# Kernel tuning notes

Hardware: AMD Instinct MI355X
Metric: run time of the kernel (lower is better)

Reference implementation:

```python
import jax, jax.numpy as jnp
import numpy as np

B, L, D_WORD, D_TIME, POS_DIM = 16, 200, 64, 56, 8
T_DIM = D_WORD + D_TIME + POS_DIM  # 128 = transformer_dim
N_HEADS, D_K, D_V = 2, 64, 64
USER_SIZE = 20000
POS_VOCAB = 1000
PAD = 0
NEG_BIG = float(-(2 ** 32) + 1)


def _layer_norm(x, g, b, eps=1e-5):
    mu = jnp.mean(x, axis=-1, keepdims=True)
    var = jnp.var(x, axis=-1, keepdims=True)
    return (x - mu) * jax.lax.rsqrt(var + eps) * g + b


def setup_inputs() -> dict:
    key = jax.random.key(0)
    ks = jax.random.split(key, 16)

    def xn(k, shape, fan):
        # xavier_normal-like scale
        std = (2.0 / (shape[0] + shape[1])) ** 0.5
        return jax.random.normal(k, shape, dtype=jnp.float32) * std

    return {
        "input_embeddings": jax.random.normal(ks[0], (B, L, D_WORD), dtype=jnp.float32),
        "time_embedding": jax.random.normal(ks[1], (B, L, D_TIME), dtype=jnp.float32),
        "inputs": jax.random.randint(ks[2], (B, L), 0, USER_SIZE, dtype=jnp.int32),
        "pos_table": jax.random.normal(ks[3], (POS_VOCAB, POS_DIM), dtype=jnp.float32) * 0.02,
        "W_q": xn(ks[4], (T_DIM, N_HEADS * D_K), 0),
        "W_k": xn(ks[5], (T_DIM, N_HEADS * D_K), 0),
        "W_v": xn(ks[6], (T_DIM, N_HEADS * D_V), 0),
        "W_o": xn(ks[7], (N_HEADS * D_V, T_DIM), 0),
        "lin1_w": xn(ks[8], (T_DIM, T_DIM), 0),
        "lin1_b": jnp.zeros((T_DIM,), dtype=jnp.float32),
        "lin2_w": xn(ks[9], (T_DIM, T_DIM), 0),
        "lin2_b": jnp.zeros((T_DIM,), dtype=jnp.float32),
        "ln_g": jnp.ones((T_DIM,), dtype=jnp.float32),
        "ln_b": jnp.zeros((T_DIM,), dtype=jnp.float32),
        "pred_w": xn(ks[10], (T_DIM, USER_SIZE), 0),
        "pred_b": jnp.zeros((USER_SIZE,), dtype=jnp.float32),
    }


def _forward(input_embeddings, time_embedding, inputs, pos_table,
             W_q, W_k, W_v, W_o, lin1_w, lin1_b, lin2_w, lin2_b,
             ln_g, ln_b, pred_w, pred_b):
    bsz, q_len, _ = input_embeddings.shape
    pad_mask = (inputs == PAD)  # (B, L) query-row padding mask

    # user_lt_attention + merger reduce to identity residual path here (eval, no extra params)
    user_embedding = input_embeddings
    order_embed = pos_table[jnp.arange(q_len)]  # (L, 8)
    order_embed = jnp.broadcast_to(order_embed[None], (bsz, q_len, POS_DIM))
    x = jnp.concatenate([user_embedding, time_embedding, order_embed], axis=-1)  # (B,L,T_DIM)

    # multi-head attention (hand-rolled, same math as TransformerBlock)
    Qh = (x @ W_q).reshape(bsz, q_len, N_HEADS, D_K).transpose(0, 2, 1, 3)  # bhqd
    Kh = (x @ W_k).reshape(bsz, q_len, N_HEADS, D_K).transpose(0, 2, 1, 3)
    Vh = (x @ W_v).reshape(bsz, q_len, N_HEADS, D_V).transpose(0, 2, 1, 3)

    temperature = D_K ** 0.5 + 1e-6
    scores = jnp.einsum('bhqd,bhkd->bhqk', Qh, Kh) / temperature
    causal = jnp.triu(jnp.ones((q_len, q_len), dtype=bool), k=1)  # (L,L)
    mask_ = causal[None, None, :, :] | pad_mask[:, None, :, None]  # causal OR query-pad rows
    scores = jnp.where(mask_, NEG_BIG, scores)
    attn = jax.nn.softmax(scores, axis=-1)
    V_att = jnp.einsum('bhqk,bhkd->bhqd', attn, Vh)
    V_att = V_att.transpose(0, 2, 1, 3).reshape(bsz, q_len, N_HEADS * D_V)
    V_att = V_att @ W_o  # (B,L,T_DIM)

    X = _layer_norm(x + V_att, ln_g, ln_b)
    ffn = jax.nn.relu(X @ lin1_w + lin1_b) @ lin2_w + lin2_b
    att_out = _layer_norm(ffn + X, ln_g, ln_b)

    pred = att_out @ pred_w + pred_b  # (B, L, USER_SIZE)

    # previous-user mask: -inf at every user id already seen at or before step i
    seqs = jnp.broadcast_to(inputs[:, None, :], (bsz, q_len, q_len))  # seqs[b,i,j]=inputs[b,j]
    tril = jnp.tril(jnp.ones((q_len, q_len), dtype=inputs.dtype))
    idx = seqs * tril  # future positions -> index 0 (matches torch tril*seqs)
    idx = jnp.concatenate([idx, jnp.zeros((bsz, q_len, 1), dtype=inputs.dtype)], axis=-1)
    bi = jnp.arange(bsz)[:, None, None]
    li = jnp.arange(q_len)[None, :, None]
    prev_mask = jnp.zeros((bsz, q_len, USER_SIZE), dtype=pred.dtype).at[bi, li, idx].set(-jnp.inf)

    return pred + prev_mask


def reference(input_embeddings, time_embedding, inputs, pos_table,
              W_q, W_k, W_v, W_o, lin1_w, lin1_b, lin2_w, lin2_b,
              ln_g, ln_b, pred_w, pred_b):
    return _forward(input_embeddings, time_embedding, inputs, pos_table,
                    W_q, W_k, W_v, W_o, lin1_w, lin1_b, lin2_w, lin2_b,
                    ln_g, ln_b, pred_w, pred_b)
```

## Files before the change

kernel.cpp:

```cpp
#include <hip/hip_runtime.h>
#include <math.h>
#include <float.h>

#define BB_ 16
#define LL_ 200
#define TD 128
#define DK 64
#define NH 2
#define USER 20000
#define ROWS (BB_ * LL_)
#define NEG_BIG (-4294967295.0f)
#define MASK_NEG (-1.0e30f)

typedef unsigned short u16;
typedef __attribute__((ext_vector_type(8))) short bf16x8;
typedef __attribute__((ext_vector_type(4))) float f32x4;

__device__ __forceinline__ u16 f2bf(float f) {
    unsigned int u = __float_as_uint(f);
    u = (u + 0x7FFFu + ((u >> 16) & 1u)) >> 16;
    return (u16)u;
}

__global__ void qkv_kernel(const float* __restrict__ emb,
                           const float* __restrict__ tim,
                           const float* __restrict__ pos,
                           const float* __restrict__ Wq,
                           const float* __restrict__ Wk,
                           const float* __restrict__ Wv,
                           float* __restrict__ x,
                           float* __restrict__ q,
                           float* __restrict__ k,
                           float* __restrict__ v) {
    int r = blockIdx.x;
    int c = threadIdx.x;
    int b = r / LL_, l = r % LL_;
    __shared__ float xr[TD];
    float xv;
    if (c < 64)        xv = emb[r * 64 + c];
    else if (c < 120)  xv = tim[r * 56 + (c - 64)];
    else               xv = pos[l * 8 + (c - 120)];
    xr[c] = xv;
    x[r * TD + c] = xv;
    __syncthreads();
    float aq = 0.f, ak = 0.f, av = 0.f;
#pragma unroll 8
    for (int kk = 0; kk < TD; ++kk) {
        float xx = xr[kk];
        aq += xx * Wq[kk * TD + c];
        ak += xx * Wk[kk * TD + c];
        av += xx * Wv[kk * TD + c];
    }
    int h = c >> 6, d = c & 63;
    int base = ((b * NH + h) * LL_ + l) * DK + d;
    q[base] = aq; k[base] = ak; v[base] = av;
}

__global__ __launch_bounds__(256) void attn_kernel(const float* __restrict__ q,
                                                   const float* __restrict__ k,
                                                   const float* __restrict__ v,
                                                   const int* __restrict__ inputs,
                                                   float* __restrict__ vatt) {
    int blk = blockIdx.x;
    int bh = blk / LL_, qi = blk % LL_;
    int b = bh >> 1, h = bh & 1;
    int t = threadIdx.x;
    int w = t >> 6;
    __shared__ float4 qrow4[DK / 4];
    __shared__ float p[256];
    __shared__ float wmax[4], wsum[4];
    __shared__ float pvred[4][DK];

    if (t < DK / 4) qrow4[t] = ((const float4*)(q + (size_t)(bh * LL_ + qi) * DK))[t];
    __syncthreads();

    bool padq = (inputs[b * LL_ + qi] == 0);
    float s = -INFINITY;
    if (t < LL_) {
        if (t > qi || padq) {
            s = NEG_BIG;
        } else {
            const float4* kr = (const float4*)(k + (size_t)(bh * LL_ + t) * DK);
            float acc = 0.f;
#pragma unroll
            for (int d4 = 0; d4 < DK / 4; ++d4) {
                float4 kv = kr[d4], qv = qrow4[d4];
                acc = fmaf(qv.x, kv.x, fmaf(qv.y, kv.y,
                      fmaf(qv.z, kv.z, fmaf(qv.w, kv.w, acc))));
            }
            s = acc / 8.000001f;
        }
    }
    float m = s;
#pragma unroll
    for (int off = 32; off >= 1; off >>= 1) m = fmaxf(m, __shfl_xor(m, off));
    if ((t & 63) == 0) wmax[w] = m;
    __syncthreads();
    float mx = fmaxf(fmaxf(wmax[0], wmax[1]), fmaxf(wmax[2], wmax[3]));

    float e = (t < LL_) ? expf(s - mx) : 0.f;
    p[t] = e;
    float ss = e;
#pragma unroll
    for (int off = 32; off >= 1; off >>= 1) ss += __shfl_xor(ss, off);
    if ((t & 63) == 0) wsum[w] = ss;
    __syncthreads();
    float inv = 1.0f / ((wsum[0] + wsum[1]) + (wsum[2] + wsum[3]));

    int d = t & 63;
    const float* vb = v + ((size_t)(bh * LL_ + w * 50)) * DK + d;
    float acc = 0.f;
#pragma unroll 10
    for (int i = 0; i < 50; ++i)
        acc = fmaf(p[w * 50 + i], vb[(size_t)i * DK], acc);
    pvred[w][d] = acc;
    __syncthreads();
    if (t < DK) {
        float r = (pvred[0][t] + pvred[1][t]) + (pvred[2][t] + pvred[3][t]);
        vatt[(size_t)(b * LL_ + qi) * TD + h * DK + t] = r * inv;
    }
}

__device__ __forceinline__ float block_ln_128(float y, float* red, int c,
                                              const float* g, const float* bb) {
    red[c] = y; __syncthreads();
    for (int st = 64; st > 0; st >>= 1) {
        if (c < st) red[c] += red[c + st];
        __syncthreads();
    }
    float mu = red[0] * (1.0f / 128.0f);
    __syncthreads();
    float d = y - mu;
    red[c] = d * d; __syncthreads();
    for (int st = 64; st > 0; st >>= 1) {
        if (c < st) red[c] += red[c + st];
        __syncthreads();
    }
    float var = red[0] * (1.0f / 128.0f);
    __syncthreads();
    return d * (1.0f / sqrtf(var + 1e-5f)) * g[c] + bb[c];
}

__global__ void mlp_kernel(const float* __restrict__ vatt,
                           const float* __restrict__ x,
                           const float* __restrict__ Wo,
                           const float* __restrict__ l1w,
                           const float* __restrict__ l1b,
                           const float* __restrict__ l2w,
                           const float* __restrict__ l2b,
                           const float* __restrict__ g,
                           const float* __restrict__ bb,
                           u16* __restrict__ att_b) {
    int r = blockIdx.x;
    int c = threadIdx.x;
    __shared__ float vr[TD], Xs[TD], h1[TD], red[TD];
    vr[c] = vatt[r * TD + c];
    __syncthreads();
    float acc = 0.f;
#pragma unroll 8
    for (int kk = 0; kk < TD; ++kk) acc += vr[kk] * Wo[kk * TD + c];
    float y = acc + x[r * TD + c];
    float Xc = block_ln_128(y, red, c, g, bb);
    Xs[c] = Xc;
    __syncthreads();
    float a1 = l1b[c];
#pragma unroll 8
    for (int kk = 0; kk < TD; ++kk) a1 += Xs[kk] * l1w[kk * TD + c];
    h1[c] = fmaxf(a1, 0.f);
    __syncthreads();
    float a2 = l2b[c];
#pragma unroll 8
    for (int kk = 0; kk < TD; ++kk) a2 += h1[kk] * l2w[kk * TD + c];
    float z = a2 + Xc;
    att_b[r * TD + c] = f2bf(block_ln_128(z, red, c, g, bb));
}

__global__ __launch_bounds__(256) void pack_w(const float* __restrict__ W,
                                              u16* __restrict__ Bp) {
    int idx = blockIdx.x * 256 + threadIdx.x;
    int kb = idx / USER;
    int n  = idx - kb * USER;
    const float* wp = W + (size_t)kb * 8 * USER + n;
    bf16x8 vv;
#pragma unroll
    for (int j = 0; j < 8; ++j) vv[j] = (short)f2bf(wp[(size_t)j * USER]);
    *(bf16x8*)(Bp + (size_t)idx * 8) = vv;
}

__global__ __launch_bounds__(256) void pred_mfma(const u16* __restrict__ Ab,
                                                 const u16* __restrict__ Bp,
                                                 const float* __restrict__ bias,
                                                 float* __restrict__ out) {
    int wave = threadIdx.x >> 6;
    int lane = threadIdx.x & 63;
    int l15 = lane & 15, l4 = lane >> 4;
    int m0 = blockIdx.y * 64;
    int n0 = blockIdx.x * 256 + wave * 64;

    f32x4 acc[4][4];
#pragma unroll
    for (int mf = 0; mf < 4; ++mf)
#pragma unroll
        for (int nf = 0; nf < 4; ++nf)
            acc[mf][nf] = (f32x4){0.f, 0.f, 0.f, 0.f};

    const u16* Aptr = Ab + (size_t)(m0 + l15) * TD + l4 * 8;

#pragma unroll
    for (int ks = 0; ks < 4; ++ks) {
        bf16x8 a[4], b[4];
#pragma unroll
        for (int mf = 0; mf < 4; ++mf)
            a[mf] = *(const bf16x8*)(Aptr + mf * 16 * TD + ks * 32);
#pragma unroll
        for (int nf = 0; nf < 4; ++nf) {
            int col = n0 + nf * 16 + l15;
            if (col >= USER) col = USER - 1;
            b[nf] = *(const bf16x8*)(Bp + ((size_t)(ks * 4 + l4) * USER + col) * 8);
        }
#pragma unroll
        for (int mf = 0; mf < 4; ++mf)
#pragma unroll
            for (int nf = 0; nf < 4; ++nf)
                acc[mf][nf] = __builtin_amdgcn_mfma_f32_16x16x32_bf16(
                    b[nf], a[mf], acc[mf][nf], 0, 0, 0);
    }

#pragma unroll
    for (int nf = 0; nf < 4; ++nf) {
        int n = n0 + nf * 16 + l4 * 4;
        if (n < USER) {
            f32x4 bw = *(const f32x4*)(bias + n);
#pragma unroll
            for (int mf = 0; mf < 4; ++mf) {
                f32x4 val = acc[mf][nf];
                val.x += bw.x; val.y += bw.y; val.z += bw.z; val.w += bw.w;
                __builtin_nontemporal_store(val,
                    (f32x4*)(out + (size_t)(m0 + mf * 16 + l15) * USER + n));
            }
        }
    }
}

__global__ void mask_kernel(const int* __restrict__ inputs, float* __restrict__ out) {
    int r = blockIdx.x;
    int b = r / LL_, i = r % LL_;
    int t = threadIdx.x;
    float* row = out + (size_t)r * USER;
    if (t == 0) row[0] = MASK_NEG;
    for (int j = t; j <= i; j += 128) {
        int u = inputs[b * LL_ + j];
        row[u] = MASK_NEG;
    }
}

extern "C" void kernel_launch(void* const* d_in, const int* in_sizes, int n_in,
                              void* d_out, int out_size, void* d_ws, size_t ws_size,
                              hipStream_t stream) {
    const float* emb   = (const float*)d_in[0];
    const float* tim   = (const float*)d_in[1];
    const int*   inp   = (const int*)  d_in[2];
    const float* pos   = (const float*)d_in[3];
    const float* Wq    = (const float*)d_in[4];
    const float* Wk    = (const float*)d_in[5];
    const float* Wv    = (const float*)d_in[6];
    const float* Wo    = (const float*)d_in[7];
    const float* l1w   = (const float*)d_in[8];
    const float* l1b   = (const float*)d_in[9];
    const float* l2w   = (const float*)d_in[10];
    const float* l2b   = (const float*)d_in[11];
    const float* g     = (const float*)d_in[12];
    const float* bbeta = (const float*)d_in[13];
    const float* predw = (const float*)d_in[14];
    const float* predb = (const float*)d_in[15];
    float* out = (float*)d_out;

    float* ws   = (float*)d_ws;
    float* x    = ws;
    float* q    = x    + ROWS * TD;
    float* k    = q    + ROWS * TD;
    float* v    = k    + ROWS * TD;
    float* vatt = v    + ROWS * TD;
    u16* att_b  = (u16*)(vatt + ROWS * TD);
    u16* Wb     = att_b + ROWS * TD;

    hipLaunchKernelGGL(qkv_kernel, dim3(ROWS), dim3(TD), 0, stream,
                       emb, tim, pos, Wq, Wk, Wv, x, q, k, v);
    hipLaunchKernelGGL(attn_kernel, dim3(BB_ * NH * LL_), dim3(256), 0, stream,
                       q, k, v, inp, vatt);
    hipLaunchKernelGGL(mlp_kernel, dim3(ROWS), dim3(TD), 0, stream,
                       vatt, x, Wo, l1w, l1b, l2w, l2b, g, bbeta, att_b);
    hipLaunchKernelGGL(pack_w, dim3(16 * USER / 256), dim3(256), 0, stream,
                       predw, Wb);
    hipLaunchKernelGGL(pred_mfma, dim3((USER + 255) / 256, ROWS / 64), dim3(256), 0, stream,
                       att_b, Wb, predb, out);
    hipLaunchKernelGGL(mask_kernel, dim3(ROWS), dim3(TD), 0, stream,
                       inp, out);
}
```

Measured before the change: 470.3 us.

## Batch QKV rows per block, store K transposed, swap pred grid order

The QKV projection now handles 8 rows per block, so each weight load is reused across 8 rows instead of 1. K is written in a transposed layout so that in the attention score loop neighbouring threads read contiguous addresses across key positions. The prediction GEMM grid is reordered so the row-tile index varies fastest, which changes which weight and activation tiles sit in cache together. The change costs more registers in the QKV kernel and gives it fewer blocks. It also assumes 8-row groups never cross a batch boundary, which holds because 200 is divisible by 8.

```diff
diff --git a/kernel.cpp b/kernel.cpp
--- a/kernel.cpp
+++ b/kernel.cpp
@@ -9,6 +9,7 @@
 #define NH 2
 #define USER 20000
 #define ROWS (BB_ * LL_)
+#define QROWS 8
 #define NEG_BIG (-4294967295.0f)
 #define MASK_NEG (-1.0e30f)
 
@@ -22,7 +23,7 @@
     return (u16)u;
 }
 
-__global__ void qkv_kernel(const float* __restrict__ emb,
+__global__ __launch_bounds__(128) void qkv_kernel(const float* __restrict__ emb,
                            const float* __restrict__ tim,
                            const float* __restrict__ pos,
                            const float* __restrict__ Wq,
@@ -30,34 +31,54 @@
                            const float* __restrict__ Wv,
                            float* __restrict__ x,
                            float* __restrict__ q,
-                           float* __restrict__ k,
+                           float* __restrict__ kT,
                            float* __restrict__ v) {
-    int r = blockIdx.x;
+    int r0 = blockIdx.x * QROWS;
     int c = threadIdx.x;
-    int b = r / LL_, l = r % LL_;
-    __shared__ float xr[TD];
-    float xv;
-    if (c < 64)        xv = emb[r * 64 + c];
-    else if (c < 120)  xv = tim[r * 56 + (c - 64)];
-    else               xv = pos[l * 8 + (c - 120)];
-    xr[c] = xv;
-    x[r * TD + c] = xv;
-    __syncthreads();
-    float aq = 0.f, ak = 0.f, av = 0.f;
+    __shared__ float xr[QROWS][TD];
+#pragma unroll
+    for (int i = 0; i < QROWS; ++i) {
+        int r = r0 + i;
+        int l = r % LL_;
+        float xv;
+        if (c < 64)        xv = emb[r * 64 + c];
+        else if (c < 120)  xv = tim[r * 56 + (c - 64)];
+        else               xv = pos[l * 8 + (c - 120)];
+        xr[i][c] = xv;
+        x[r * TD + c] = xv;
+    }
+    __syncthreads();
+    float aq[QROWS], ak[QROWS], av[QROWS];
+#pragma unroll
+    for (int i = 0; i < QROWS; ++i) { aq[i] = 0.f; ak[i] = 0.f; av[i] = 0.f; }
 #pragma unroll 8
     for (int kk = 0; kk < TD; ++kk) {
-        float xx = xr[kk];
-        aq += xx * Wq[kk * TD + c];
-        ak += xx * Wk[kk * TD + c];
-        av += xx * Wv[kk * TD + c];
+        float wq = Wq[kk * TD + c], wk = Wk[kk * TD + c], wv = Wv[kk * TD + c];
+#pragma unroll
+        for (int i = 0; i < QROWS; ++i) {
+            float xx = xr[i][kk];
+            aq[i] = fmaf(xx, wq, aq[i]);
+            ak[i] = fmaf(xx, wk, ak[i]);
+            av[i] = fmaf(xx, wv, av[i]);
+        }
     }
     int h = c >> 6, d = c & 63;
-    int base = ((b * NH + h) * LL_ + l) * DK + d;
-    q[base] = aq; k[base] = ak; v[base] = av;
+    int b = r0 / LL_, l0 = r0 % LL_;
+    int bh = b * NH + h;
+#pragma unroll
+    for (int i = 0; i < QROWS; ++i) {
+        q[(bh * LL_ + l0 + i) * DK + d] = aq[i];
+        v[(bh * LL_ + l0 + i) * DK + d] = av[i];
+    }
+    float4 k0 = {ak[0], ak[1], ak[2], ak[3]};
+    float4 k1 = {ak[4], ak[5], ak[6], ak[7]};
+    float* kp = kT + (size_t)(bh * DK + d) * LL_ + l0;
+    *(float4*)kp = k0;
+    *(float4*)(kp + 4) = k1;
 }
 
 __global__ __launch_bounds__(256) void attn_kernel(const float* __restrict__ q,
-                                                   const float* __restrict__ k,
+                                                   const float* __restrict__ kT,
                                                    const float* __restrict__ v,
                                                    const int* __restrict__ inputs,
                                                    float* __restrict__ vatt) {
@@ -66,12 +87,12 @@
     int b = bh >> 1, h = bh & 1;
     int t = threadIdx.x;
     int w = t >> 6;
-    __shared__ float4 qrow4[DK / 4];
+    __shared__ float qrow[DK];
     __shared__ float p[256];
     __shared__ float wmax[4], wsum[4];
     __shared__ float pvred[4][DK];
 
-    if (t < DK / 4) qrow4[t] = ((const float4*)(q + (size_t)(bh * LL_ + qi) * DK))[t];
+    if (t < DK) qrow[t] = q[(size_t)(bh * LL_ + qi) * DK + t];
     __syncthreads();
 
     bool padq = (inputs[b * LL_ + qi] == 0);
@@ -80,14 +101,11 @@
         if (t > qi || padq) {
             s = NEG_BIG;
         } else {
-            const float4* kr = (const float4*)(k + (size_t)(bh * LL_ + t) * DK);
+            const float* kp = kT + (size_t)bh * DK * LL_ + t;
             float acc = 0.f;
-#pragma unroll
-            for (int d4 = 0; d4 < DK / 4; ++d4) {
-                float4 kv = kr[d4], qv = qrow4[d4];
-                acc = fmaf(qv.x, kv.x, fmaf(qv.y, kv.y,
-                      fmaf(qv.z, kv.z, fmaf(qv.w, kv.w, acc))));
-            }
+#pragma unroll 8
+            for (int d = 0; d < DK; ++d)
+                acc = fmaf(qrow[d], kp[(size_t)d * LL_], acc);
             s = acc / 8.000001f;
         }
     }
@@ -194,8 +212,8 @@
     int wave = threadIdx.x >> 6;
     int lane = threadIdx.x & 63;
     int l15 = lane & 15, l4 = lane >> 4;
-    int m0 = blockIdx.y * 64;
-    int n0 = blockIdx.x * 256 + wave * 64;
+    int m0 = blockIdx.x * 64;
+    int n0 = blockIdx.y * 256 + wave * 64;
 
     f32x4 acc[4][4];
 #pragma unroll
@@ -278,21 +296,21 @@
     float* ws   = (float*)d_ws;
     float* x    = ws;
     float* q    = x    + ROWS * TD;
-    float* k    = q    + ROWS * TD;
-    float* v    = k    + ROWS * TD;
+    float* kT   = q    + ROWS * TD;
+    float* v    = kT   + ROWS * TD;
     float* vatt = v    + ROWS * TD;
     u16* att_b  = (u16*)(vatt + ROWS * TD);
     u16* Wb     = att_b + ROWS * TD;
 
-    hipLaunchKernelGGL(qkv_kernel, dim3(ROWS), dim3(TD), 0, stream,
-                       emb, tim, pos, Wq, Wk, Wv, x, q, k, v);
+    hipLaunchKernelGGL(qkv_kernel, dim3(ROWS / QROWS), dim3(TD), 0, stream,
+                       emb, tim, pos, Wq, Wk, Wv, x, q, kT, v);
     hipLaunchKernelGGL(attn_kernel, dim3(BB_ * NH * LL_), dim3(256), 0, stream,
-                       q, k, v, inp, vatt);
+                       q, kT, v, inp, vatt);
     hipLaunchKernelGGL(mlp_kernel, dim3(ROWS), dim3(TD), 0, stream,
                        vatt, x, Wo, l1w, l1b, l2w, l2b, g, bbeta, att_b);
     hipLaunchKernelGGL(pack_w, dim3(16 * USER / 256), dim3(256), 0, stream,
                        predw, Wb);
-    hipLaunchKernelGGL(pred_mfma, dim3((USER + 255) / 256, ROWS / 64), dim3(256), 0, stream,
+    hipLaunchKernelGGL(pred_mfma, dim3(ROWS / 64, (USER + 255) / 256), dim3(256), 0, stream,
                        att_b, Wb, predb, out);
     hipLaunchKernelGGL(mask_kernel, dim3(ROWS), dim3(TD), 0, stream,
                        inp, out);
```

Measured after the change: 499.9 us. 6.3% more time.
